# Performance work log

Measured on AMD Instinct MI355X. Metric: run time of the kernel, lower is better.

The kernel has to match this reference:

```python
import jax, jax.numpy as jnp
import numpy as np

K = 5
BASE_LAMBDA = 0.05
BASE_DELTA = 0.01
ITERS = 3
STEP = 0.2
FUSION_SCALE = 2.0
EPS = 1e-8


def _param_sets():
    # Deterministic (jitter_strength=0) version of SASConfig._generate_param_sets.
    # View 0 is identity; views 1..K-1 get linearly spaced lambda and coupled delta.
    lmin, lmax = BASE_LAMBDA * 0.5, BASE_LAMBDA * 1.5
    lams, deltas = [], []
    for i in range(K - 1):
        lam = lmin + (lmax - lmin) * i / max(1, K - 2)
        lams.append(lam)
        deltas.append(BASE_DELTA * np.sqrt(lam / (BASE_LAMBDA + 1e-8)))
    return jnp.asarray(lams, jnp.float32), jnp.asarray(deltas, jnp.float32)


def _huber_tv(x, lam, delta):
    # Anisotropic Huber-TV diffusion, skip_clamp=True (artifact denoising path).
    # x: [B,C,H,W]
    xd = x
    for _ in range(ITERS):
        dx = jnp.pad(xd[:, :, :, 1:] - xd[:, :, :, :-1], ((0, 0), (0, 0), (0, 0), (0, 1)))
        dy = jnp.pad(xd[:, :, 1:, :] - xd[:, :, :-1, :], ((0, 0), (0, 0), (0, 1), (0, 0)))
        gx = dx / (delta + jnp.abs(dx))
        gy = dy / (delta + jnp.abs(dy))
        # divergence with replicated first element (div[...,0] = g[...,0])
        div_x = gx - jnp.pad(gx[:, :, :, :-1], ((0, 0), (0, 0), (0, 0), (1, 0)))
        div_y = gy - jnp.pad(gy[:, :, :-1, :], ((0, 0), (0, 0), (1, 0), (0, 0)))
        xd = xd - STEP * (xd - x - lam * (div_x + div_y))
    return xd


def setup_inputs() -> dict:
    key = jax.random.key(0)
    x = jax.random.normal(key, (32, 3, 256, 256), dtype=jnp.float32)
    return {"x": x}


def reference(x):
    B = x.shape[0]
    # torch.median over flattened |artifact| (lower median for even count)
    flat = jnp.abs(x).reshape(B, -1)
    n = flat.shape[1]
    scale = jnp.sort(flat, axis=1)[:, (n - 1) // 2].reshape(B, 1, 1, 1) + 1e-8

    lams, deltas = _param_sets()
    xn = x / scale
    denoised = jax.vmap(lambda l, d: _huber_tv(xn, l, d))(lams, deltas)  # [K-1,B,C,H,W]
    arts = jnp.concatenate([x[None], denoised * scale[None]], axis=0)  # [K,B,C,H,W]

    # Robust MAD-weighted fusion (K=5 is odd, jnp.median == torch.median over dim 0)
    med = jnp.median(arts, axis=0)
    dev = jnp.abs(arts - med[None])
    mad = jnp.median(dev, axis=0)
    mad = jnp.maximum(mad, 0.1 * mad.mean())
    w = jnp.exp(-dev / (FUSION_SCALE * mad[None]))
    fused = (w * arts).sum(axis=0) / (w.sum(axis=0) + EPS)
    return fused
```

## Files before the change

kernel.cpp:

```cpp
#include <hip/hip_runtime.h>
#include <math.h>

typedef unsigned int u32;
typedef unsigned long long u64;

#define NPIX 6291456


__device__ __forceinline__ float med3f(float a, float b, float c) {
    return fmaxf(fminf(a, b), fminf(fmaxf(a, b), c));
}
__device__ __forceinline__ float med5f(float a0, float a1, float a2, float a3, float a4) {
    float mn01 = fminf(a0, a1), mx01 = fmaxf(a0, a1);
    float mn34 = fminf(a3, a4), mx34 = fmaxf(a3, a4);
    return med3f(a2, fmaxf(mn01, mn34), fminf(mx01, mx34));
}
__device__ __forceinline__ u32 packbf(float lo, float hi) {
    u32 a = __float_as_uint(lo), b = __float_as_uint(hi);
    a = (a + 0x7FFFu + ((a >> 16) & 1u)) >> 16;
    b = (b + 0x7FFFu + ((b >> 16) & 1u)) >> 16;
    return a | (b << 16);
}

__device__ __forceinline__ u32 scan1024(u32 v, u32* wtot) {
    int lane = threadIdx.x & 63, wid = threadIdx.x >> 6;
    u32 inc = v;
    #pragma unroll
    for (int off = 1; off < 64; off <<= 1) {
        u32 o = __shfl_up(inc, off);
        if (lane >= off) inc += o;
    }
    __syncthreads();
    if (lane == 63) wtot[wid] = inc;
    __syncthreads();
    for (int w = 0; w < wid; ++w) inc += wtot[w];
    return inc;
}


__global__ __launch_bounds__(1024) void hist_kernel(
        const float* __restrict__ x, u32* __restrict__ hist,
        float* __restrict__ madsum) {
    __shared__ u32 lh[16400];
    int b = blockIdx.x >> 3, s = blockIdx.x & 7, t = threadIdx.x;
    uint4 z = make_uint4(0u, 0u, 0u, 0u);
    #pragma unroll
    for (int j = 0; j < 4; ++j) ((uint4*)lh)[t + j * 1024] = z;
    if (t < 4) ((uint4*)lh)[4096 + t] = z;
    __syncthreads();
    const float4* xb = (const float4*)(x + (size_t)b * 196608 + s * 24576);
    u32 sub = (u32)(t & 3) * 4100u;
    #pragma unroll
    for (int i = 0; i < 6; ++i) {
        float4 v = xb[t + i * 1024];
        atomicAdd(&lh[sub + (__float_as_uint(fabsf(v.x)) >> 19)], 1u);
        atomicAdd(&lh[sub + (__float_as_uint(fabsf(v.y)) >> 19)], 1u);
        atomicAdd(&lh[sub + (__float_as_uint(fabsf(v.z)) >> 19)], 1u);
        atomicAdd(&lh[sub + (__float_as_uint(fabsf(v.w)) >> 19)], 1u);
    }
    __syncthreads();
    u32 a0 = 0, a1 = 0, a2 = 0, a3 = 0;
    #pragma unroll
    for (int sb = 0; sb < 4; ++sb) {
        uint4 hv = *(const uint4*)&lh[sb * 4100u + (u32)t * 4u];
        a0 += hv.x; a1 += hv.y; a2 += hv.z; a3 += hv.w;
    }
    u32* hb = hist + ((size_t)b * 8 + s) * 4096;
    ((uint4*)hb)[t] = make_uint4(a0, a1, a2, a3);
    if (s == 0 && t == 0 && b == 0) *madsum = 0.0f;
}


__global__ __launch_bounds__(1024) void extract_kernel(
        const float* __restrict__ x, const u32* __restrict__ hist,
        u32* __restrict__ members, u32* __restrict__ scount,
        u32* __restrict__ selBin, u32* __restrict__ selKr) {
    __shared__ u32 sbuf[8192];
    __shared__ u32 wtot[16];
    __shared__ u32 sBin, lcnt;
    int b = blockIdx.x >> 3, s = blockIdx.x & 7, t = threadIdx.x, lane = t & 63;
    if (t == 0) lcnt = 0u;
    const u32* hb = hist + (size_t)b * 32768;
    u32 s4[4] = {0u, 0u, 0u, 0u};
    #pragma unroll
    for (int sl = 0; sl < 8; ++sl) {
        uint4 h4 = ((const uint4*)(hb + sl * 4096))[t];
        s4[0] += h4.x; s4[1] += h4.y; s4[2] += h4.z; s4[3] += h4.w;
    }
    u32 sum = s4[0] + s4[1] + s4[2] + s4[3];
    u32 inc = scan1024(sum, wtot);
    u32 exc = inc - sum;
    u32 k = 98303u;
    if (exc <= k && k < inc) {
        u32 kr = k - exc;
        int j = 0;
        while (kr >= s4[j]) { kr -= s4[j]; ++j; }
        sBin = (u32)(t * 4 + j);
        if (s == 0) { selBin[b] = (u32)(t * 4 + j); selKr[b] = kr; }
    }
    __syncthreads();
    u32 bin = sBin;
    const float4* xb = (const float4*)(x + (size_t)b * 196608 + s * 24576);
    #pragma unroll 2
    for (int i = 0; i < 6; ++i) {
        float4 v = xb[t + i * 1024];
        float vv[4] = {v.x, v.y, v.z, v.w};
        #pragma unroll
        for (int e = 0; e < 4; ++e) {
            u32 bits = __float_as_uint(fabsf(vv[e]));
            bool is = (bits >> 19) == bin;
            u64 ball = __ballot(is);
            if (ball) {
                u32 cnt = (u32)__popcll(ball);
                u32 base = 0;
                if (lane == 0) base = atomicAdd(&lcnt, cnt);
                base = __shfl(base, 0);
                if (is) {
                    u32 p = base + (u32)__popcll(ball & ((1ull << lane) - 1ull));
                    if (p < 8192u) sbuf[p] = bits & 0x7FFFFu;
                }
            }
        }
    }
    __syncthreads();
    u32 cnt = lcnt; if (cnt > 8192u) cnt = 8192u;
    u32* mb = members + ((size_t)b * 8 + s) * 8192;
    for (u32 i = (u32)t; i < cnt; i += 1024u) mb[i] = sbuf[i];
    if (t == 0) scount[b * 8 + s] = cnt;
}


__global__ __launch_bounds__(1024) void select_kernel(
        const u32* __restrict__ scount, const u32* __restrict__ members,
        const u32* __restrict__ selBin, const u32* __restrict__ selKr,
        float* __restrict__ scale) {
    __shared__ u32 sbuf[8192];
    __shared__ u32 h[128];
    __shared__ u32 wtot[16];
    __shared__ u32 sPfx, sK;
    int b = blockIdx.x, t = threadIdx.x;
    u32 c[8], off[8], tot = 0u;
    #pragma unroll
    for (int s = 0; s < 8; ++s) {
        c[s] = scount[b * 8 + s];
        off[s] = tot;
        tot += c[s];
    }
    #pragma unroll
    for (int s = 0; s < 8; ++s) {
        const u32* mb = members + ((size_t)b * 8 + s) * 8192;
        for (u32 i = (u32)t; i < c[s]; i += 1024u) {
            u32 p = off[s] + i;
            if (p < 8192u) sbuf[p] = mb[i];
        }
    }
    u32 m = tot; if (m > 8192u) m = 8192u;
    if (t == 0) { sPfx = 0u; sK = selKr[b]; }
    __syncthreads();
    const int shf[3] = {12, 6, 0};
    const int wd[3]  = {7, 6, 6};
    const u32 msk[3] = {127u, 63u, 63u};
    #pragma unroll 1
    for (int rd = 0; rd < 3; ++rd) {
        u32 pfx = sPfx, k2 = sK;
        if (t < 128) h[t] = 0u;
        __syncthreads();
        for (u32 i = (u32)t; i < m; i += 1024u) {
            u32 v = sbuf[i];
            if ((v >> (shf[rd] + wd[rd])) == pfx)
                atomicAdd(&h[(v >> shf[rd]) & msk[rd]], 1u);
        }
        __syncthreads();
        u32 nb = msk[rd] + 1u;
        u32 cc = ((u32)t < nb) ? h[t] : 0u;
        u32 inc2 = scan1024(cc, wtot);
        u32 exc2 = inc2 - cc;
        if ((u32)t < nb && exc2 <= k2 && k2 < inc2) {
            sPfx = (pfx << wd[rd]) | (u32)t;
            sK = k2 - exc2;
        }
        __syncthreads();
    }
    if (t == 0)
        scale[b] = __uint_as_float((selBin[b] << 19) | sPfx) + 1e-8f;
}


__device__ __forceinline__ float dpp_shl1(float v) {
    return __uint_as_float((u32)__builtin_amdgcn_update_dpp(
        0, (int)__float_as_uint(v), 0x130, 0xF, 0xF, true));
}
__device__ __forceinline__ float dpp_shr1(float v) {
    return __uint_as_float((u32)__builtin_amdgcn_update_dpp(
        0, (int)__float_as_uint(v), 0x138, 0xF, 0xF, true));
}
__device__ __forceinline__ float hub(float d, float del) {
    return d * __builtin_amdgcn_rcpf(del + fabsf(d));
}
__device__ __forceinline__ float upd(float b, float xn, float dv, float lam) {
    float t = fmaf(-lam, dv, b - xn);
    return fmaf(-0.2f, t, b);
}

__device__ __forceinline__ float4 stage4(float4 B, float4 C, float4 xn, float4& gyp,
                                         int row, float mR3, float mL0,
                                         float lam, float del) {
    float mr = (row < 255) ? 1.f : 0.f;
    float m0 = (row == 0) ? 0.f : 1.f;
    float gy0 = hub(C.x - B.x, del) * mr;
    float gy1 = hub(C.y - B.y, del) * mr;
    float gy2 = hub(C.z - B.z, del) * mr;
    float gy3 = hub(C.w - B.w, del) * mr;
    float dv0 = gy0 - gyp.x * m0;
    float dv1 = gy1 - gyp.y * m0;
    float dv2 = gy2 - gyp.z * m0;
    float dv3 = gy3 - gyp.w * m0;
    gyp.x = gy0; gyp.y = gy1; gyp.z = gy2; gyp.w = gy3;
    float B0n = dpp_shl1(B.x);
    float g01 = hub(B.y - B.x, del);
    float g12 = hub(B.z - B.y, del);
    float g23 = hub(B.w - B.z, del);
    float g3n = hub(B0n - B.w, del) * mR3;
    float gp  = dpp_shr1(g3n) * mL0;
    float4 o;
    o.x = upd(B.x, xn.x, (g01 - gp)  + dv0, lam);
    o.y = upd(B.y, xn.y, (g12 - g01) + dv1, lam);
    o.z = upd(B.z, xn.z, (g23 - g12) + dv2, lam);
    o.w = upd(B.w, xn.w, (g3n - g23) + dv3, lam);
    return o;
}

__global__ __launch_bounds__(256, 6) void denoise_kernel(
        const float* __restrict__ x, const float* __restrict__ scale,
        u32* __restrict__ arts, float* __restrict__ madsum,
        float4 lam4, float4 del4) {
    __shared__ float sex[5][256];
    __shared__ float red[4];
    int t = threadIdx.x, lane = t & 63, wid = t >> 6;
    int img = blockIdx.x >> 4;
    int seg = blockIdx.x & 15;
    float sc = scale[img / 3];
    float lam = ((wid == 0) ? lam4.x : (wid == 1) ? lam4.y : (wid == 2) ? lam4.z : lam4.w) * sc;
    float del = ((wid == 0) ? del4.x : (wid == 1) ? del4.y : (wid == 2) ? del4.z : del4.w) * sc;
    float mR3 = (lane == 63) ? 0.f : 1.f;
    float mL0 = (lane == 0) ? 0.f : 1.f;
    const float4* xp = (const float4*)(x + (size_t)img * 65536) + lane;
    u32* ap = arts + (size_t)wid * (NPIX / 2) + (size_t)img * 32768 + lane * 2;

    float4 z4 = {0.f, 0.f, 0.f, 0.f};
    float4 cur1 = z4, cur2 = z4, gyp1 = z4, gyp2 = z4, gyp3 = z4;
    float4 n0 = z4, n1 = z4, n2 = z4;
    int out_lo = seg * 16, out_hi = out_lo + 15;
    int rs = (out_lo >= 3) ? out_lo - 3 : 0;
    int rend = out_hi + 3;
    float msum = 0.f;

    float4 nl = xp[rs << 6];
    for (int r = rs; r <= rend; ++r) {
        int rn = (r + 1 <= 255) ? r + 1 : 255;
        float4 nxt = xp[rn << 6];
        int r1 = r - 1, r2 = r - 2, r3 = r - 3;
        float4 x1 = stage4(n0,   nl, n0, gyp1, r1, mR3, mL0, lam, del);
        float4 x2 = stage4(cur1, x1, n1, gyp2, r2, mR3, mL0, lam, del);
        float4 x3 = stage4(cur2, x2, n2, gyp3, r3, mR3, mL0, lam, del);
        cur1 = x1; cur2 = x2;
        if (r3 >= out_lo) {
            uint2 pk;
            pk.x = packbf(x3.x, x3.y);
            pk.y = packbf(x3.z, x3.w);
            *(uint2*)(ap + (r3 << 7)) = pk;
            *(float4*)&sex[wid + 1][lane * 4] = x3;
            if (wid == 0) *(float4*)&sex[0][lane * 4] = n2;
            __syncthreads();
            int c = wid * 64 + lane;
            float a0 = sex[0][c], a1 = sex[1][c], a2 = sex[2][c],
                  a3 = sex[3][c], a4 = sex[4][c];
            float med = med5f(a0, a1, a2, a3, a4);
            msum += med5f(fabsf(a0 - med), fabsf(a1 - med), fabsf(a2 - med),
                          fabsf(a3 - med), fabsf(a4 - med));
            __syncthreads();
        }
        n2 = n1; n1 = n0; n0 = nl;
        nl = nxt;
    }
    #pragma unroll
    for (int off = 32; off > 0; off >>= 1) msum += __shfl_down(msum, off);
    if (lane == 0) red[wid] = msum;
    __syncthreads();
    if (t == 0) atomicAdd(madsum, red[0] + red[1] + red[2] + red[3]);
}


__global__ __launch_bounds__(256) void fuse_kernel(
        const float* __restrict__ x, const u32* __restrict__ artsU,
        const float* __restrict__ madsum, float* __restrict__ out) {
    int t = blockIdx.x * 256 + threadIdx.x;
    float floorv = 0.1f * (*madsum) * (1.0f / 6291456.0f);
    float2 xv = ((const float2*)x)[t];
    u32 p0 = artsU[t];
    u32 p1 = artsU[t + NPIX / 2];
    u32 p2 = artsU[t + NPIX];
    u32 p3 = artsU[t + 3 * (NPIX / 2)];
    float2 o;
#define FUSE1(res, A0, SH) { \
        float a0 = A0; \
        float a1 = __uint_as_float(SH(p0)), a2 = __uint_as_float(SH(p1)); \
        float a3 = __uint_as_float(SH(p2)), a4 = __uint_as_float(SH(p3)); \
        float med = med5f(a0, a1, a2, a3, a4); \
        float d0 = fabsf(a0 - med), d1 = fabsf(a1 - med), d2 = fabsf(a2 - med); \
        float d3 = fabsf(a3 - med), d4 = fabsf(a4 - med); \
        float mad = med5f(d0, d1, d2, d3, d4); \
        float mm = fmaxf(mad, floorv); \
        float inv = 0.5f / mm; \
        float w0 = __expf(-d0 * inv), w1 = __expf(-d1 * inv), w2 = __expf(-d2 * inv); \
        float w3 = __expf(-d3 * inv), w4 = __expf(-d4 * inv); \
        float swt = w0 + w1 + w2 + w3 + w4; \
        float sva = fmaf(w0, a0, fmaf(w1, a1, fmaf(w2, a2, fmaf(w3, a3, w4 * a4)))); \
        res = sva / (swt + 1e-8f); \
    }
#define LO16(u) ((u) << 16)
#define HI16(u) ((u) & 0xFFFF0000u)
    FUSE1(o.x, xv.x, LO16);
    FUSE1(o.y, xv.y, HI16);
#undef FUSE1
#undef LO16
#undef HI16
    ((float2*)out)[t] = o;
}


extern "C" void kernel_launch(void* const* d_in, const int* in_sizes, int n_in,
                              void* d_out, int out_size, void* d_ws, size_t ws_size,
                              hipStream_t stream) {
    const float* x = (const float*)d_in[0];
    float* out = (float*)d_out;
    char* ws = (char*)d_ws;
    float* scale  = (float*)ws;
    float* madsum = (float*)(ws + 128);
    u32* selBin   = (u32*)(ws + 384);
    u32* selKr    = (u32*)(ws + 512);
    u32* artsU    = (u32*)(ws + 1024);
    u32* hist     = artsU;
    u32* members  = artsU + (size_t)32 * 8 * 4096;
    u32* scount   = members + (size_t)32 * 8 * 8192;

    hist_kernel<<<256, 1024, 0, stream>>>(x, hist, madsum);
    extract_kernel<<<256, 1024, 0, stream>>>(x, hist, members, scount, selBin, selKr);
    select_kernel<<<32, 1024, 0, stream>>>(scount, members, selBin, selKr, scale);

    float lamf[4], delf[4];
    for (int i = 0; i < 4; ++i) {
        double lam = 0.025 + 0.05 * (double)i / 3.0;
        lamf[i] = (float)lam;
        delf[i] = (float)(0.01 * sqrt(lam / (0.05 + 1e-8)));
    }
    float4 lam4 = make_float4(lamf[0], lamf[1], lamf[2], lamf[3]);
    float4 del4 = make_float4(delf[0], delf[1], delf[2], delf[3]);

    denoise_kernel<<<1536, 256, 0, stream>>>(x, scale, artsU, madsum, lam4, del4);
    fuse_kernel<<<12288, 256, 0, stream>>>(x, artsU, madsum, out);
}
```

Baseline: 178.4 us.

## Double-buffer denoise LDS exchange, halve halo overhead, widen fuse to 4 pixels

The denoise kernel now double-buffers its shared-memory exchange on row parity, which lets it drop the second barrier per output row. Segments grow from 16 to 32 rows, halving the redundant halo recomputation but also halving the grid to 768 blocks. The fuse kernel handles four pixels per thread using float4 and uint2 loads, halving its grid. The larger segments reduce parallelism and the wider fuse raises register pressure.

```diff
diff --git a/kernel.cpp b/kernel.cpp
--- a/kernel.cpp
+++ b/kernel.cpp
@@ -234,11 +234,11 @@
         const float* __restrict__ x, const float* __restrict__ scale,
         u32* __restrict__ arts, float* __restrict__ madsum,
         float4 lam4, float4 del4) {
-    __shared__ float sex[5][256];
+    __shared__ float sex[2][5][256];
     __shared__ float red[4];
     int t = threadIdx.x, lane = t & 63, wid = t >> 6;
-    int img = blockIdx.x >> 4;
-    int seg = blockIdx.x & 15;
+    int img = blockIdx.x >> 3;
+    int seg = blockIdx.x & 7;
     float sc = scale[img / 3];
     float lam = ((wid == 0) ? lam4.x : (wid == 1) ? lam4.y : (wid == 2) ? lam4.z : lam4.w) * sc;
     float del = ((wid == 0) ? del4.x : (wid == 1) ? del4.y : (wid == 2) ? del4.z : del4.w) * sc;
@@ -250,7 +250,7 @@
     float4 z4 = {0.f, 0.f, 0.f, 0.f};
     float4 cur1 = z4, cur2 = z4, gyp1 = z4, gyp2 = z4, gyp3 = z4;
     float4 n0 = z4, n1 = z4, n2 = z4;
-    int out_lo = seg * 16, out_hi = out_lo + 15;
+    int out_lo = seg * 32, out_hi = out_lo + 31;
     int rs = (out_lo >= 3) ? out_lo - 3 : 0;
     int rend = out_hi + 3;
     float msum = 0.f;
@@ -269,16 +269,16 @@
             pk.x = packbf(x3.x, x3.y);
             pk.y = packbf(x3.z, x3.w);
             *(uint2*)(ap + (r3 << 7)) = pk;
-            *(float4*)&sex[wid + 1][lane * 4] = x3;
-            if (wid == 0) *(float4*)&sex[0][lane * 4] = n2;
+            int pb = r3 & 1;
+            *(float4*)&sex[pb][wid + 1][lane * 4] = x3;
+            if (wid == 0) *(float4*)&sex[pb][0][lane * 4] = n2;
             __syncthreads();
             int c = wid * 64 + lane;
-            float a0 = sex[0][c], a1 = sex[1][c], a2 = sex[2][c],
-                  a3 = sex[3][c], a4 = sex[4][c];
+            float a0 = sex[pb][0][c], a1 = sex[pb][1][c], a2 = sex[pb][2][c],
+                  a3 = sex[pb][3][c], a4 = sex[pb][4][c];
             float med = med5f(a0, a1, a2, a3, a4);
             msum += med5f(fabsf(a0 - med), fabsf(a1 - med), fabsf(a2 - med),
                           fabsf(a3 - med), fabsf(a4 - med));
-            __syncthreads();
         }
         n2 = n1; n1 = n0; n0 = nl;
         nl = nxt;
@@ -296,16 +296,16 @@
         const float* __restrict__ madsum, float* __restrict__ out) {
     int t = blockIdx.x * 256 + threadIdx.x;
     float floorv = 0.1f * (*madsum) * (1.0f / 6291456.0f);
-    float2 xv = ((const float2*)x)[t];
-    u32 p0 = artsU[t];
-    u32 p1 = artsU[t + NPIX / 2];
-    u32 p2 = artsU[t + NPIX];
-    u32 p3 = artsU[t + 3 * (NPIX / 2)];
-    float2 o;
-#define FUSE1(res, A0, SH) { \
+    float4 xv = ((const float4*)x)[t];
+    uint2 q0 = ((const uint2*)(artsU))[t];
+    uint2 q1 = ((const uint2*)(artsU + NPIX / 2))[t];
+    uint2 q2 = ((const uint2*)(artsU + NPIX))[t];
+    uint2 q3 = ((const uint2*)(artsU + 3 * (NPIX / 2)))[t];
+    float4 o;
+#define FUSE1(res, A0, U0, U1, U2, U3, SH) { \
         float a0 = A0; \
-        float a1 = __uint_as_float(SH(p0)), a2 = __uint_as_float(SH(p1)); \
-        float a3 = __uint_as_float(SH(p2)), a4 = __uint_as_float(SH(p3)); \
+        float a1 = __uint_as_float(SH(U0)), a2 = __uint_as_float(SH(U1)); \
+        float a3 = __uint_as_float(SH(U2)), a4 = __uint_as_float(SH(U3)); \
         float med = med5f(a0, a1, a2, a3, a4); \
         float d0 = fabsf(a0 - med), d1 = fabsf(a1 - med), d2 = fabsf(a2 - med); \
         float d3 = fabsf(a3 - med), d4 = fabsf(a4 - med); \
@@ -320,12 +320,14 @@
     }
 #define LO16(u) ((u) << 16)
 #define HI16(u) ((u) & 0xFFFF0000u)
-    FUSE1(o.x, xv.x, LO16);
-    FUSE1(o.y, xv.y, HI16);
+    FUSE1(o.x, xv.x, q0.x, q1.x, q2.x, q3.x, LO16);
+    FUSE1(o.y, xv.y, q0.x, q1.x, q2.x, q3.x, HI16);
+    FUSE1(o.z, xv.z, q0.y, q1.y, q2.y, q3.y, LO16);
+    FUSE1(o.w, xv.w, q0.y, q1.y, q2.y, q3.y, HI16);
 #undef FUSE1
 #undef LO16
 #undef HI16
-    ((float2*)out)[t] = o;
+    ((float4*)out)[t] = o;
 }
 
 
@@ -357,6 +359,6 @@
     float4 lam4 = make_float4(lamf[0], lamf[1], lamf[2], lamf[3]);
     float4 del4 = make_float4(delf[0], delf[1], delf[2], delf[3]);
 
-    denoise_kernel<<<1536, 256, 0, stream>>>(x, scale, artsU, madsum, lam4, del4);
-    fuse_kernel<<<12288, 256, 0, stream>>>(x, artsU, madsum, out);
-}
+    denoise_kernel<<<768, 256, 0, stream>>>(x, scale, artsU, madsum, lam4, del4);
+    fuse_kernel<<<6144, 256, 0, stream>>>(x, artsU, madsum, out);
+}
```

Measured after the change: 177.8 us. No clear change (-0.3%).
